# Performance work log

Measured on AMD Instinct MI355X. Metric: run time of the kernel, lower is better.

The kernel has to match this reference:

```python
import jax, jax.numpy as jnp
import numpy as np

TEMPERATURE = 0.07
B, D, NUM_CLASSES = 8192, 256, 100

def setup_inputs() -> dict:
    key = jax.random.key(0)
    kz, kl = jax.random.split(key)
    z = jax.random.normal(kz, (B, D), dtype=jnp.float32)
    z = z / jnp.linalg.norm(z, axis=-1, keepdims=True)  # unit-norm embeddings keep exp(logits/T) finite
    labels = jax.random.randint(kl, (B,), 0, NUM_CLASSES, dtype=jnp.int64)
    return {"z": z, "labels": labels}

def reference(z, labels):
    n = z.shape[0]
    same = labels[:, None] == labels[None, :]              # [B, B] bool
    eye = jnp.eye(n, dtype=bool)
    pos_mask = (same & ~eye).astype(z.dtype)               # positives exclude self
    neg_mask = (~same).astype(z.dtype)                     # mask == 0 entries
    exp_logits = jnp.exp(z @ z.T / TEMPERATURE)            # [B, B]
    sum_neg = jnp.sum(exp_logits * neg_mask, axis=1)       # [B]
    # per positive pair: -log(e_ij / (e_ij + sum_neg_i))
    pair_loss = jnp.log1p(sum_neg[:, None] / exp_logits)   # = -log(e/(e+sn)), stable form
    pos_cnt = jnp.sum(pos_mask, axis=1)                    # [B]
    row_loss = jnp.sum(pair_loss * pos_mask, axis=1) / jnp.maximum(pos_cnt, 1.0)
    valid = (pos_cnt > 0).astype(z.dtype)
    n_valid = jnp.sum(valid)
    loss = jnp.where(n_valid > 0,
                     jnp.sum(row_loss * valid) / jnp.maximum(n_valid, 1.0),
                     jnp.zeros((), z.dtype))
    return loss
```

## Files before the change

### kernel.cpp

```cpp
#include <hip/hip_runtime.h>
#include <hip/hip_bf16.h>


#define BN 8192
#define DD 256
#define INV_T (1.0f / 0.07f)
#define CAPI 256
#define CAP 160

typedef __attribute__((ext_vector_type(8))) __bf16 bf16x8;
typedef __attribute__((ext_vector_type(4))) float f32x4;

typedef const __attribute__((address_space(1))) void gas_void;
typedef __attribute__((address_space(3))) void las_void;

static __device__ __forceinline__ void gld_lds16(const void* g, void* l) {
    __builtin_amdgcn_global_load_lds((gas_void*)g, (las_void*)l, 16, 0, 0);
}

static __device__ __forceinline__ unsigned short f2bf(float f) {
    unsigned int u = __builtin_bit_cast(unsigned int, f);
    u = (u + 0x7FFFu + ((u >> 16) & 1u)) >> 16;
    return (unsigned short)u;
}

__global__ __launch_bounds__(256) void k_prep(const float* __restrict__ z,
                                              unsigned short* __restrict__ zbf,
                                              float* __restrict__ sn,
                                              int* __restrict__ cls_cnt) {
    const int gid = blockIdx.x * 256 + threadIdx.x;
    const float4* z4 = (const float4*)z;
    float4 v0 = z4[gid * 2 + 0];
    float4 v1 = z4[gid * 2 + 1];
    unsigned short r[8];
    r[0] = f2bf(v0.x); r[1] = f2bf(v0.y); r[2] = f2bf(v0.z); r[3] = f2bf(v0.w);
    r[4] = f2bf(v1.x); r[5] = f2bf(v1.y); r[6] = f2bf(v1.z); r[7] = f2bf(v1.w);
    ((uint4*)zbf)[gid] = *(const uint4*)r;
    if (gid < BN) sn[gid] = 0.f;
    if (blockIdx.x == 0 && threadIdx.x < 100) cls_cnt[threadIdx.x] = 0;
}

__global__ __launch_bounds__(256) void k_bucket(const int* __restrict__ labels,
                                                int* __restrict__ cls_cnt,
                                                int* __restrict__ cls_idx) {
    const int gid = blockIdx.x * 256 + threadIdx.x;
    if (gid < BN) {
        const int c = labels[gid];
        const int slot = atomicAdd(&cls_cnt[c], 1);
        if (slot < CAPI) cls_idx[c * CAPI + slot] = gid;
    }
}

__global__ __launch_bounds__(256) void k_passA(const unsigned short* __restrict__ zbf,
                                               float* __restrict__ sn) {
    __shared__ char Bb[2][32768];
    __shared__ float cs_lds[64];

    const int tid = threadIdx.x;
    const int w = tid >> 6, lane = tid & 63;
    const int l15 = lane & 15, lk = lane >> 4;
    const int p = blockIdx.x >> 4, q = blockIdx.x & 15;
    const int r0 = p, r1 = 63 - p;
    const int n0 = 128 - 2 * r0;
    const int jlo = (130 * q) >> 4, jhi = (130 * (q + 1)) >> 4;
    const char* zb = (const char*)zbf;

    auto cstepOf = [&](int j, int& s, int& c) {
        if (j < n0) { s = r0; c = 2 * r0 + j; }
        else        { s = r1; c = 2 * r1 + (j - n0); }
    };
    auto stage = [&](int buf, int c) {
        const char* gB = zb + (size_t)c * 64 * 512;
        char* lb = Bb[buf];
#pragma unroll
        for (int qq = 0; qq < 8; ++qq) {
            const int s = (qq * 256 + tid) * 16;
            const int col = s >> 9, koff = s & 511;
            const int ksrc = koff ^ ((col & 7) << 4);
            gld_lds16(gB + (size_t)col * 512 + ksrc, lb + s);
        }
    };

    bf16x8 a[2][8];
    float snp[2][4];
    int igr[2][4];

    auto flush = [&]() {
#pragma unroll
        for (int m = 0; m < 2; ++m)
#pragma unroll
            for (int rr = 0; rr < 4; ++rr) {
                float v = snp[m][rr];
                v += __shfl_xor(v, 1, 64);
                v += __shfl_xor(v, 2, 64);
                v += __shfl_xor(v, 4, 64);
                v += __shfl_xor(v, 8, 64);
                if (l15 == 0) atomicAdd(&sn[igr[m][rr]], v);
            }
    };

    int s0, c0_; cstepOf(jlo, s0, c0_);
    stage(0, c0_);
    if (tid < 64) cs_lds[tid] = 0.f;

    int cur = -1, buf = 0;
    __syncthreads();

    for (int jj = jlo; jj < jhi; ++jj) {
        int s, c; cstepOf(jj, s, c);
        const bool diag = ((c >> 1) == s);
        if (s != cur) {
            if (cur >= 0) flush();
#pragma unroll
            for (int m = 0; m < 2; ++m) {
                const char* ap = zb + (size_t)(s * 128 + w * 32 + m * 16 + l15) * 512 + lk * 16;
#pragma unroll
                for (int kf = 0; kf < 8; ++kf) a[m][kf] = *(const bf16x8*)(ap + kf * 64);
#pragma unroll
                for (int rr = 0; rr < 4; ++rr) {
                    snp[m][rr] = 0.f;
                    igr[m][rr] = s * 128 + w * 32 + m * 16 + lk * 4 + rr;
                }
            }
            cur = s;
        }
        if (jj + 1 < jhi) { int s2, c2; cstepOf(jj + 1, s2, c2); stage(buf ^ 1, c2); }

        const char* bp0 = Bb[buf];
#pragma unroll
        for (int n = 0; n < 4; ++n) {
            const int col = n * 16 + l15;
            const char* bp = bp0 + col * 512;
            const int sw = (col & 7) << 4;
            bf16x8 b[8];
#pragma unroll
            for (int kf = 0; kf < 8; ++kf)
                b[kf] = *(const bf16x8*)(bp + ((lk * 16 + kf * 64) ^ sw));
            const int jg = c * 64 + col;
            float cs_n = 0.f;
#pragma unroll
            for (int m = 0; m < 2; ++m) {
                f32x4 acc = {};
#pragma unroll
                for (int kf = 0; kf < 8; ++kf)
                    acc = __builtin_amdgcn_mfma_f32_16x16x32_bf16(a[m][kf], b[kf], acc, 0, 0, 0);
#pragma unroll
                for (int rr = 0; rr < 4; ++rr) {
                    float e = __expf(acc[rr] * INV_T);
                    if (diag && igr[m][rr] == jg) e = 0.f;
                    snp[m][rr] += e;
                    cs_n += e;
                }
            }
            cs_n += __shfl_xor(cs_n, 16, 64);
            cs_n += __shfl_xor(cs_n, 32, 64);
            if (lane < 16) atomicAdd(&cs_lds[col], cs_n);
        }
        __syncthreads();
        if (tid < 64) {
            const float v = cs_lds[tid];
            if (!diag) atomicAdd(&sn[c * 64 + tid], v);
            cs_lds[tid] = 0.f;
        }
        __syncthreads();
        buf ^= 1;
    }
    flush();
}

__global__ __launch_bounds__(256) void k_passB(const unsigned short* __restrict__ zbf,
                                               const float* __restrict__ sn,
                                               const int* __restrict__ cls_cnt,
                                               const int* __restrict__ cls_idx,
                                               float* __restrict__ row_loss,
                                               float* __restrict__ validf) {
    __shared__ char Zc[CAP * 512];
    __shared__ int glist[CAP];
    __shared__ float snl[CAP];
    __shared__ float sums[CAP];

    const int c = blockIdx.x;
    const int sy = blockIdx.y;
    const int tid = threadIdx.x;
    const int w = tid >> 6, lane = tid & 63;
    const int l15 = lane & 15, lk = lane >> 4;
    const char* zb = (const char*)zbf;

    const int n_c = min(cls_cnt[c], CAP);
    const int nt = (n_c + 15) >> 4;
    const int rows_p = nt * 16;

    if (tid < n_c) glist[tid] = cls_idx[c * CAPI + tid];
    __syncthreads();

    for (int e = w; e < rows_p; e += 4) {
        uint2 v = {0u, 0u};
        if (e < n_c) v = *(const uint2*)(zb + (size_t)glist[e] * 512 + lane * 8);
        *(uint2*)(Zc + e * 512 + ((lane * 8) ^ ((e & 7) << 4))) = v;
    }
    __syncthreads();

    for (int mi = w; mi < nt; mi += 4) {
        const int rowA = mi * 16 + l15;
        bf16x8 a[8];
        const char* ap = Zc + rowA * 512;
        const int swa = (rowA & 7) << 4;
#pragma unroll
        for (int kf = 0; kf < 8; ++kf)
            a[kf] = *(const bf16x8*)(ap + ((lk * 16 + kf * 64) ^ swa));
        float sp[4] = {};
        for (int nj = 0; nj < nt; ++nj) {
            const int colB = nj * 16 + l15;
            bf16x8 b[8];
            const char* bp = Zc + colB * 512;
            const int swb = (colB & 7) << 4;
#pragma unroll
            for (int kf = 0; kf < 8; ++kf)
                b[kf] = *(const bf16x8*)(bp + ((lk * 16 + kf * 64) ^ swb));
            f32x4 acc = {};
#pragma unroll
            for (int kf = 0; kf < 8; ++kf)
                acc = __builtin_amdgcn_mfma_f32_16x16x32_bf16(a[kf], b[kf], acc, 0, 0, 0);
#pragma unroll
            for (int rr = 0; rr < 4; ++rr) {
                const int i = mi * 16 + lk * 4 + rr;
                const float e = __expf(acc[rr] * INV_T);
                sp[rr] += (colB < n_c && i != colB) ? e : 0.f;
            }
        }
#pragma unroll
        for (int rr = 0; rr < 4; ++rr) {
            float v = sp[rr];
            v += __shfl_xor(v, 1, 64);
            v += __shfl_xor(v, 2, 64);
            v += __shfl_xor(v, 4, 64);
            v += __shfl_xor(v, 8, 64);
            if (l15 == 0) sums[mi * 16 + lk * 4 + rr] = v;
        }
    }
    __syncthreads();
    if (tid < n_c) snl[tid] = sn[glist[tid]] - sums[tid];
    __syncthreads();

    const int mi = sy + 4 * w;
    if (mi < nt) {
        const int rowA = mi * 16 + l15;
        bf16x8 a[8];
        const char* ap = Zc + rowA * 512;
        const int swa = (rowA & 7) << 4;
#pragma unroll
        for (int kf = 0; kf < 8; ++kf)
            a[kf] = *(const bf16x8*)(ap + ((lk * 16 + kf * 64) ^ swa));
        float sneg[4];
#pragma unroll
        for (int rr = 0; rr < 4; ++rr) {
            const int i = mi * 16 + lk * 4 + rr;
            sneg[rr] = (i < n_c) ? snl[i] : 0.f;
        }
        float sp[4] = {};
        for (int nj = 0; nj < nt; ++nj) {
            const int colB = nj * 16 + l15;
            bf16x8 b[8];
            const char* bp = Zc + colB * 512;
            const int swb = (colB & 7) << 4;
#pragma unroll
            for (int kf = 0; kf < 8; ++kf)
                b[kf] = *(const bf16x8*)(bp + ((lk * 16 + kf * 64) ^ swb));
            f32x4 acc = {};
#pragma unroll
            for (int kf = 0; kf < 8; ++kf)
                acc = __builtin_amdgcn_mfma_f32_16x16x32_bf16(a[kf], b[kf], acc, 0, 0, 0);
#pragma unroll
            for (int rr = 0; rr < 4; ++rr) {
                const int i = mi * 16 + lk * 4 + rr;
                const float t = log1pf(sneg[rr] * __expf(-acc[rr] * INV_T));
                sp[rr] += (colB < n_c && i != colB) ? t : 0.f;
            }
        }
#pragma unroll
        for (int rr = 0; rr < 4; ++rr) {
            float v = sp[rr];
            v += __shfl_xor(v, 1, 64);
            v += __shfl_xor(v, 2, 64);
            v += __shfl_xor(v, 4, 64);
            v += __shfl_xor(v, 8, 64);
            const int i = mi * 16 + lk * 4 + rr;
            if (l15 == 0 && i < n_c) {
                const int gi = glist[i];
                row_loss[gi] = (n_c > 1) ? v / (float)(n_c - 1) : 0.f;
                validf[gi] = (n_c > 1) ? 1.f : 0.f;
            }
        }
    }
}

__global__ __launch_bounds__(1024) void k_final(const float* __restrict__ row_loss,
                                                const float* __restrict__ validf,
                                                float* __restrict__ out) {
    __shared__ float ls[16], vs[16];
    float l = 0.f, v = 0.f;
    for (int r = threadIdx.x; r < BN; r += 1024) {
        const float f = validf[r];
        l += row_loss[r] * f;
        v += f;
    }
#pragma unroll
    for (int m = 1; m < 64; m <<= 1) {
        l += __shfl_xor(l, m, 64);
        v += __shfl_xor(v, m, 64);
    }
    if ((threadIdx.x & 63) == 0) { ls[threadIdx.x >> 6] = l; vs[threadIdx.x >> 6] = v; }
    __syncthreads();
    if (threadIdx.x == 0) {
        float L = 0.f, V = 0.f;
        for (int i = 0; i < 16; ++i) { L += ls[i]; V += vs[i]; }
        out[0] = (V > 0.f) ? L / fmaxf(V, 1.f) : 0.f;
    }
}

extern "C" void kernel_launch(void* const* d_in, const int* in_sizes, int n_in,
                              void* d_out, int out_size, void* d_ws, size_t ws_size,
                              hipStream_t stream) {
    const float* z      = (const float*)d_in[0];
    const int*   labels = (const int*)d_in[1];
    float* out = (float*)d_out;

    char* ws = (char*)d_ws;
    unsigned short* zbf = (unsigned short*)ws;
    size_t off = (size_t)BN * DD * sizeof(unsigned short);
    float* sn      = (float*)(ws + off);  off += BN * sizeof(float);
    float* rl      = (float*)(ws + off);  off += BN * sizeof(float);
    float* vf      = (float*)(ws + off);  off += BN * sizeof(float);
    int*   cls_cnt = (int*)(ws + off);    off += 1024;
    int*   cls_idx = (int*)(ws + off);    off += 100 * CAPI * sizeof(int);

    k_prep  <<<1024, 256, 0, stream>>>(z, zbf, sn, cls_cnt);
    k_bucket<<<32, 256, 0, stream>>>(labels, cls_cnt, cls_idx);
    k_passA <<<512, 256, 0, stream>>>(zbf, sn);
    k_passB <<<dim3(100, 4), 256, 0, stream>>>(zbf, sn, cls_cnt, cls_idx, rl, vf);
    k_final <<<1, 1024, 0, stream>>>(rl, vf, out);
}
```

Measured before the change: 95.61 us.

## Retile Gram pass to 128x128 LDS tiles and fuse loss reduction into class pass

The negative-sum pass moves from 128x64 tiles with double-buffered column staging to 128x128 symmetric tiles. The A rows are staged once through LDS per row block, and each wave computes a 64x64 sub-tile with four accumulators, which raises MFMA reuse per B fragment. The work is now single-buffered with extra barriers, so global loads no longer overlap compute. The per-class loss kernel runs one 512-thread block per class, stages rows with global_load_lds, and accumulates the loss and valid count atomically into a global accumulator. This removes the per-row output arrays and the 8192-element final reduction.

```diff
diff --git a/kernel.cpp b/kernel.cpp
--- a/kernel.cpp
+++ b/kernel.cpp
@@ -27,7 +27,8 @@
 __global__ __launch_bounds__(256) void k_prep(const float* __restrict__ z,
                                               unsigned short* __restrict__ zbf,
                                               float* __restrict__ sn,
-                                              int* __restrict__ cls_cnt) {
+                                              int* __restrict__ cls_cnt,
+                                              float* __restrict__ gacc) {
     const int gid = blockIdx.x * 256 + threadIdx.x;
     const float4* z4 = (const float4*)z;
     float4 v0 = z4[gid * 2 + 0];
@@ -37,7 +38,10 @@
     r[4] = f2bf(v1.x); r[5] = f2bf(v1.y); r[6] = f2bf(v1.z); r[7] = f2bf(v1.w);
     ((uint4*)zbf)[gid] = *(const uint4*)r;
     if (gid < BN) sn[gid] = 0.f;
-    if (blockIdx.x == 0 && threadIdx.x < 100) cls_cnt[threadIdx.x] = 0;
+    if (blockIdx.x == 0) {
+        if (threadIdx.x < 100) cls_cnt[threadIdx.x] = 0;
+        if (threadIdx.x < 2) gacc[threadIdx.x] = 0.f;
+    }
 }
 
 __global__ __launch_bounds__(256) void k_bucket(const int* __restrict__ labels,
@@ -51,43 +55,53 @@
     }
 }
 
-__global__ __launch_bounds__(256) void k_passA(const unsigned short* __restrict__ zbf,
-                                               float* __restrict__ sn) {
-    __shared__ char Bb[2][32768];
-    __shared__ float cs_lds[64];
+__global__ __launch_bounds__(256, 2) void k_passA(const unsigned short* __restrict__ zbf,
+                                                  float* __restrict__ sn) {
+    __shared__ char Bb[65536];
+    __shared__ float cs_lds[128];
 
     const int tid = threadIdx.x;
     const int w = tid >> 6, lane = tid & 63;
     const int l15 = lane & 15, lk = lane >> 4;
+    const int wrow = w >> 1, wcol = w & 1;
     const int p = blockIdx.x >> 4, q = blockIdx.x & 15;
-    const int r0 = p, r1 = 63 - p;
-    const int n0 = 128 - 2 * r0;
-    const int jlo = (130 * q) >> 4, jhi = (130 * (q + 1)) >> 4;
+    const int r1 = 63 - p, n0 = 64 - p;
+    const int jlo = (65 * q) >> 4, jhi = (65 * (q + 1)) >> 4;
     const char* zb = (const char*)zbf;
 
-    auto cstepOf = [&](int j, int& s, int& c) {
-        if (j < n0) { s = r0; c = 2 * r0 + j; }
-        else        { s = r1; c = 2 * r1 + (j - n0); }
+    auto Jof = [&](int j) { return (j < n0) ? p + j : r1 + (j - n0); };
+
+    auto stageTile = [&](int rowblk) {
+#pragma unroll
+        for (int cI = 0; cI < 16; ++cI) {
+            const int s = (cI * 256 + tid) * 16;
+            const int row = s >> 9, koff = s & 511;
+            gld_lds16(zb + ((size_t)(rowblk * 128 + row)) * 512 + (koff ^ ((row & 7) << 4)),
+                      (char*)Bb + s);
+        }
     };
-    auto stage = [&](int buf, int c) {
-        const char* gB = zb + (size_t)c * 64 * 512;
-        char* lb = Bb[buf];
-#pragma unroll
-        for (int qq = 0; qq < 8; ++qq) {
-            const int s = (qq * 256 + tid) * 16;
-            const int col = s >> 9, koff = s & 511;
-            const int ksrc = koff ^ ((col & 7) << 4);
-            gld_lds16(gB + (size_t)col * 512 + ksrc, lb + s);
+
+    bf16x8 a[4][8];
+    auto readA = [&]() {
+#pragma unroll
+        for (int m = 0; m < 4; ++m) {
+            const int row = wrow * 64 + m * 16 + l15;
+            const int sw = (row & 7) << 4;
+#pragma unroll
+            for (int kf = 0; kf < 8; ++kf)
+                a[m][kf] = *(const bf16x8*)(Bb + row * 512 + ((lk * 16 + kf * 64) ^ sw));
         }
     };
 
-    bf16x8 a[2][8];
-    float snp[2][4];
-    int igr[2][4];
-
-    auto flush = [&]() {
-#pragma unroll
-        for (int m = 0; m < 2; ++m)
+    float snp[4][4];
+#pragma unroll
+    for (int m = 0; m < 4; ++m)
+#pragma unroll
+        for (int rr = 0; rr < 4; ++rr) snp[m][rr] = 0.f;
+
+    auto flushRows = [&](int s) {
+#pragma unroll
+        for (int m = 0; m < 4; ++m)
 #pragma unroll
             for (int rr = 0; rr < 4; ++rr) {
                 float v = snp[m][rr];
@@ -95,92 +109,90 @@
                 v += __shfl_xor(v, 2, 64);
                 v += __shfl_xor(v, 4, 64);
                 v += __shfl_xor(v, 8, 64);
-                if (l15 == 0) atomicAdd(&sn[igr[m][rr]], v);
+                if (l15 == 0)
+                    atomicAdd(&sn[s * 128 + wrow * 64 + m * 16 + lk * 4 + rr], v);
+                snp[m][rr] = 0.f;
             }
     };
 
-    int s0, c0_; cstepOf(jlo, s0, c0_);
-    stage(0, c0_);
-    if (tid < 64) cs_lds[tid] = 0.f;
-
-    int cur = -1, buf = 0;
-    __syncthreads();
-
-    for (int jj = jlo; jj < jhi; ++jj) {
-        int s, c; cstepOf(jj, s, c);
-        const bool diag = ((c >> 1) == s);
-        if (s != cur) {
-            if (cur >= 0) flush();
-#pragma unroll
-            for (int m = 0; m < 2; ++m) {
-                const char* ap = zb + (size_t)(s * 128 + w * 32 + m * 16 + l15) * 512 + lk * 16;
-#pragma unroll
-                for (int kf = 0; kf < 8; ++kf) a[m][kf] = *(const bf16x8*)(ap + kf * 64);
+    int sCur = (jlo < n0) ? p : r1;
+
+    stageTile(sCur);
+    if (tid < 128) cs_lds[tid] = 0.f;
+    __syncthreads();
+    readA();
+    __syncthreads();
+    stageTile(Jof(jlo));
+    __syncthreads();
+
+    for (int j = jlo; j < jhi; ++j) {
+        const int Jt = Jof(j);
+        const bool diag = (Jt == sCur);
+        const int myrow0 = wrow * 64;
+        const int mycol = wcol * 64 + l15;
+
+#pragma unroll
+        for (int n = 0; n < 4; ++n) {
+            const int col = wcol * 64 + n * 16 + l15;
+            const int swb = (col & 7) << 4;
+            bf16x8 bfr[8];
+#pragma unroll
+            for (int kf = 0; kf < 8; ++kf)
+                bfr[kf] = *(const bf16x8*)(Bb + col * 512 + ((lk * 16 + kf * 64) ^ swb));
+            f32x4 accm[4] = {};
+#pragma unroll
+            for (int kf = 0; kf < 8; ++kf)
+#pragma unroll
+                for (int m = 0; m < 4; ++m)
+                    accm[m] = __builtin_amdgcn_mfma_f32_16x16x32_bf16(a[m][kf], bfr[kf], accm[m], 0, 0, 0);
+            float csn = 0.f;
+#pragma unroll
+            for (int m = 0; m < 4; ++m)
 #pragma unroll
                 for (int rr = 0; rr < 4; ++rr) {
-                    snp[m][rr] = 0.f;
-                    igr[m][rr] = s * 128 + w * 32 + m * 16 + lk * 4 + rr;
+                    float e = __expf(accm[m][rr] * INV_T);
+                    if (diag && (myrow0 + m * 16 + lk * 4 + rr) == (n * 16 + mycol)) e = 0.f;
+                    snp[m][rr] += e;
+                    csn += e;
                 }
+            csn += __shfl_xor(csn, 16, 64);
+            csn += __shfl_xor(csn, 32, 64);
+            if (!diag && lane < 16) atomicAdd(&cs_lds[wcol * 64 + n * 16 + l15], csn);
+        }
+        __syncthreads();
+        if (!diag && tid < 128) {
+            atomicAdd(&sn[Jt * 128 + tid], cs_lds[tid]);
+            cs_lds[tid] = 0.f;
+        }
+        if (j + 1 < jhi) {
+            const int sN = (j + 1 < n0) ? p : r1;
+            if (sN != sCur) {
+                flushRows(sCur);
+                stageTile(sN);
+                __syncthreads();
+                readA();
+                __syncthreads();
+                sCur = sN;
             }
-            cur = s;
-        }
-        if (jj + 1 < jhi) { int s2, c2; cstepOf(jj + 1, s2, c2); stage(buf ^ 1, c2); }
-
-        const char* bp0 = Bb[buf];
-#pragma unroll
-        for (int n = 0; n < 4; ++n) {
-            const int col = n * 16 + l15;
-            const char* bp = bp0 + col * 512;
-            const int sw = (col & 7) << 4;
-            bf16x8 b[8];
-#pragma unroll
-            for (int kf = 0; kf < 8; ++kf)
-                b[kf] = *(const bf16x8*)(bp + ((lk * 16 + kf * 64) ^ sw));
-            const int jg = c * 64 + col;
-            float cs_n = 0.f;
-#pragma unroll
-            for (int m = 0; m < 2; ++m) {
-                f32x4 acc = {};
-#pragma unroll
-                for (int kf = 0; kf < 8; ++kf)
-                    acc = __builtin_amdgcn_mfma_f32_16x16x32_bf16(a[m][kf], b[kf], acc, 0, 0, 0);
-#pragma unroll
-                for (int rr = 0; rr < 4; ++rr) {
-                    float e = __expf(acc[rr] * INV_T);
-                    if (diag && igr[m][rr] == jg) e = 0.f;
-                    snp[m][rr] += e;
-                    cs_n += e;
-                }
-            }
-            cs_n += __shfl_xor(cs_n, 16, 64);
-            cs_n += __shfl_xor(cs_n, 32, 64);
-            if (lane < 16) atomicAdd(&cs_lds[col], cs_n);
+            stageTile(Jof(j + 1));
         }
         __syncthreads();
-        if (tid < 64) {
-            const float v = cs_lds[tid];
-            if (!diag) atomicAdd(&sn[c * 64 + tid], v);
-            cs_lds[tid] = 0.f;
-        }
-        __syncthreads();
-        buf ^= 1;
-    }
-    flush();
-}
-
-__global__ __launch_bounds__(256) void k_passB(const unsigned short* __restrict__ zbf,
+    }
+    flushRows(sCur);
+}
+
+__global__ __launch_bounds__(512) void k_passB(const unsigned short* __restrict__ zbf,
                                                const float* __restrict__ sn,
                                                const int* __restrict__ cls_cnt,
                                                const int* __restrict__ cls_idx,
-                                               float* __restrict__ row_loss,
-                                               float* __restrict__ validf) {
+                                               float* __restrict__ gacc) {
     __shared__ char Zc[CAP * 512];
     __shared__ int glist[CAP];
     __shared__ float snl[CAP];
     __shared__ float sums[CAP];
+    __shared__ float blkL;
 
     const int c = blockIdx.x;
-    const int sy = blockIdx.y;
     const int tid = threadIdx.x;
     const int w = tid >> 6, lane = tid & 63;
     const int l15 = lane & 15, lk = lane >> 4;
@@ -190,33 +202,33 @@
     const int nt = (n_c + 15) >> 4;
     const int rows_p = nt * 16;
 
-    if (tid < n_c) glist[tid] = cls_idx[c * CAPI + tid];
-    __syncthreads();
-
-    for (int e = w; e < rows_p; e += 4) {
-        uint2 v = {0u, 0u};
-        if (e < n_c) v = *(const uint2*)(zb + (size_t)glist[e] * 512 + lane * 8);
-        *(uint2*)(Zc + e * 512 + ((lane * 8) ^ ((e & 7) << 4))) = v;
-    }
-    __syncthreads();
-
-    for (int mi = w; mi < nt; mi += 4) {
+    if (tid < CAP) glist[tid] = (tid < n_c) ? cls_idx[c * CAPI + tid] : 0;
+    if (tid == 0) blkL = 0.f;
+    __syncthreads();
+
+    for (int e2 = w * 2; e2 < rows_p; e2 += 16) {
+        const int row = e2 + (lane >> 5);
+        const int cb = (lane & 31) * 16;
+        gld_lds16(zb + (size_t)glist[row] * 512 + (cb ^ ((row & 7) << 4)),
+                  (char*)Zc + e2 * 512);
+    }
+    __syncthreads();
+
+    for (int mi = w; mi < nt; mi += 8) {
         const int rowA = mi * 16 + l15;
+        const int swa = (rowA & 7) << 4;
         bf16x8 a[8];
-        const char* ap = Zc + rowA * 512;
-        const int swa = (rowA & 7) << 4;
 #pragma unroll
         for (int kf = 0; kf < 8; ++kf)
-            a[kf] = *(const bf16x8*)(ap + ((lk * 16 + kf * 64) ^ swa));
+            a[kf] = *(const bf16x8*)(Zc + rowA * 512 + ((lk * 16 + kf * 64) ^ swa));
         float sp[4] = {};
         for (int nj = 0; nj < nt; ++nj) {
             const int colB = nj * 16 + l15;
+            const int swb = (colB & 7) << 4;
             bf16x8 b[8];
-            const char* bp = Zc + colB * 512;
-            const int swb = (colB & 7) << 4;
-#pragma unroll
-            for (int kf = 0; kf < 8; ++kf)
-                b[kf] = *(const bf16x8*)(bp + ((lk * 16 + kf * 64) ^ swb));
+#pragma unroll
+            for (int kf = 0; kf < 8; ++kf)
+                b[kf] = *(const bf16x8*)(Zc + colB * 512 + ((lk * 16 + kf * 64) ^ swb));
             f32x4 acc = {};
 #pragma unroll
             for (int kf = 0; kf < 8; ++kf)
@@ -239,18 +251,16 @@
         }
     }
     __syncthreads();
-    if (tid < n_c) snl[tid] = sn[glist[tid]] - sums[tid];
-    __syncthreads();
-
-    const int mi = sy + 4 * w;
-    if (mi < nt) {
+    if (tid < CAP) snl[tid] = (tid < n_c) ? sn[glist[tid]] - sums[tid] : 0.f;
+    __syncthreads();
+
+    for (int mi = w; mi < nt; mi += 8) {
         const int rowA = mi * 16 + l15;
+        const int swa = (rowA & 7) << 4;
         bf16x8 a[8];
-        const char* ap = Zc + rowA * 512;
-        const int swa = (rowA & 7) << 4;
 #pragma unroll
         for (int kf = 0; kf < 8; ++kf)
-            a[kf] = *(const bf16x8*)(ap + ((lk * 16 + kf * 64) ^ swa));
+            a[kf] = *(const bf16x8*)(Zc + rowA * 512 + ((lk * 16 + kf * 64) ^ swa));
         float sneg[4];
 #pragma unroll
         for (int rr = 0; rr < 4; ++rr) {
@@ -260,12 +270,11 @@
         float sp[4] = {};
         for (int nj = 0; nj < nt; ++nj) {
             const int colB = nj * 16 + l15;
+            const int swb = (colB & 7) << 4;
             bf16x8 b[8];
-            const char* bp = Zc + colB * 512;
-            const int swb = (colB & 7) << 4;
-#pragma unroll
-            for (int kf = 0; kf < 8; ++kf)
-                b[kf] = *(const bf16x8*)(bp + ((lk * 16 + kf * 64) ^ swb));
+#pragma unroll
+            for (int kf = 0; kf < 8; ++kf)
+                b[kf] = *(const bf16x8*)(Zc + colB * 512 + ((lk * 16 + kf * 64) ^ swb));
             f32x4 acc = {};
 #pragma unroll
             for (int kf = 0; kf < 8; ++kf)
@@ -285,35 +294,20 @@
             v += __shfl_xor(v, 4, 64);
             v += __shfl_xor(v, 8, 64);
             const int i = mi * 16 + lk * 4 + rr;
-            if (l15 == 0 && i < n_c) {
-                const int gi = glist[i];
-                row_loss[gi] = (n_c > 1) ? v / (float)(n_c - 1) : 0.f;
-                validf[gi] = (n_c > 1) ? 1.f : 0.f;
-            }
-        }
-    }
-}
-
-__global__ __launch_bounds__(1024) void k_final(const float* __restrict__ row_loss,
-                                                const float* __restrict__ validf,
-                                                float* __restrict__ out) {
-    __shared__ float ls[16], vs[16];
-    float l = 0.f, v = 0.f;
-    for (int r = threadIdx.x; r < BN; r += 1024) {
-        const float f = validf[r];
-        l += row_loss[r] * f;
-        v += f;
-    }
-#pragma unroll
-    for (int m = 1; m < 64; m <<= 1) {
-        l += __shfl_xor(l, m, 64);
-        v += __shfl_xor(v, m, 64);
-    }
-    if ((threadIdx.x & 63) == 0) { ls[threadIdx.x >> 6] = l; vs[threadIdx.x >> 6] = v; }
-    __syncthreads();
+            if (l15 == 0 && i < n_c && n_c > 1)
+                atomicAdd(&blkL, v / (float)(n_c - 1));
+        }
+    }
+    __syncthreads();
+    if (tid == 0 && n_c > 1) {
+        atomicAdd(&gacc[0], blkL);
+        atomicAdd(&gacc[1], (float)n_c);
+    }
+}
+
+__global__ void k_final(const float* __restrict__ gacc, float* __restrict__ out) {
     if (threadIdx.x == 0) {
-        float L = 0.f, V = 0.f;
-        for (int i = 0; i < 16; ++i) { L += ls[i]; V += vs[i]; }
+        const float L = gacc[0], V = gacc[1];
         out[0] = (V > 0.f) ? L / fmaxf(V, 1.f) : 0.f;
     }
 }
@@ -329,14 +323,13 @@
     unsigned short* zbf = (unsigned short*)ws;
     size_t off = (size_t)BN * DD * sizeof(unsigned short);
     float* sn      = (float*)(ws + off);  off += BN * sizeof(float);
-    float* rl      = (float*)(ws + off);  off += BN * sizeof(float);
-    float* vf      = (float*)(ws + off);  off += BN * sizeof(float);
     int*   cls_cnt = (int*)(ws + off);    off += 1024;
     int*   cls_idx = (int*)(ws + off);    off += 100 * CAPI * sizeof(int);
-
-    k_prep  <<<1024, 256, 0, stream>>>(z, zbf, sn, cls_cnt);
+    float* gacc    = (float*)(ws + off);  off += 2 * sizeof(float);
+
+    k_prep  <<<1024, 256, 0, stream>>>(z, zbf, sn, cls_cnt, gacc);
     k_bucket<<<32, 256, 0, stream>>>(labels, cls_cnt, cls_idx);
     k_passA <<<512, 256, 0, stream>>>(zbf, sn);
-    k_passB <<<dim3(100, 4), 256, 0, stream>>>(zbf, sn, cls_cnt, cls_idx, rl, vf);
-    k_final <<<1, 1024, 0, stream>>>(rl, vf, out);
-}
+    k_passB <<<100, 512, 0, stream>>>(zbf, sn, cls_cnt, cls_idx, gacc);
+    k_final <<<1, 64, 0, stream>>>(gacc, out);
+}
```

Measured after the change: 111.7 us. +16.8%, slower.
